# Performance work log

Hardware: AMD Instinct MI355X
Metric: run time of the kernel (lower is better)

## Reference

```python
import jax, jax.numpy as jnp
import numpy as np

# tinygemm asymmetric int4 convention
QUANT_MIN, QUANT_MAX = 0, 15
MID_POINT = (QUANT_MAX + QUANT_MIN + 1) / 2.0  # 8.0
OUT_F, IN_F, GROUP = 8192, 8192, 128
M_TOKENS = 64


def setup_inputs() -> dict:
    key = jax.random.key(0)
    kx, kw = jax.random.split(key)
    x = jax.random.normal(kx, (M_TOKENS, IN_F), dtype=jnp.float32)
    # Materialize quantized params exactly as quantize_weight_tinygemm does.
    w = jax.random.normal(kw, (OUT_F, IN_F), dtype=jnp.float32) * 0.02
    ng = IN_F // GROUP
    wg = w.reshape(OUT_F, ng, GROUP)
    min_val = wg.min(axis=2)
    max_val = wg.max(axis=2)
    scale = jnp.maximum((max_val - min_val) / float(QUANT_MAX - QUANT_MIN), 1.1920929e-7)
    zero_point = min_val + scale * MID_POINT
    min_val_recon = zero_point - scale * MID_POINT
    q = jnp.clip(jnp.round((wg - min_val_recon[..., None]) / scale[..., None]),
                 QUANT_MIN, QUANT_MAX).astype(jnp.int32)
    int_data = q.reshape(OUT_F, IN_F)  # values in [0, 15]
    # tinygemm layout: (n_groups, out_features, 2) with [..., 0]=scale, [..., 1]=zero_point
    scale_and_zero = jnp.stack([scale, zero_point], axis=-1).transpose(1, 0, 2)
    return {"x": x, "int_data": int_data, "scale_and_zero": scale_and_zero}


def reference(x, int_data, scale_and_zero):
    # Dequant: w = (q - MID_POINT) * scale + zero_point, per group of GROUP along in_features.
    ng = IN_F // GROUP
    q = int_data.reshape(OUT_F, ng, GROUP).astype(x.dtype)
    scale = scale_and_zero[..., 0].T[:, :, None]       # (OUT_F, ng, 1)
    zero_point = scale_and_zero[..., 1].T[:, :, None]  # (OUT_F, ng, 1)
    w = ((q - MID_POINT) * scale + zero_point).reshape(OUT_F, IN_F)
    return x @ w.T  # (M, OUT_F)
```

## Files before the change

kernel.cpp:

```cpp
#include <hip/hip_runtime.h>


#define OUT_F 8192
#define IN_F  8192
#define M_TOK 64
#define GROUP 128
#define BN    128
#define KSPLIT 16
#define KR    (IN_F / KSPLIT)

typedef short short8 __attribute__((ext_vector_type(8)));
typedef float f32x4  __attribute__((ext_vector_type(4)));
typedef int   int4v  __attribute__((ext_vector_type(4)));

__device__ __forceinline__ int pack_bf2(float lo, float hi) {
    unsigned ul = __float_as_uint(lo) + 0x8000u;
    unsigned uh = __float_as_uint(hi) + 0x8000u;
    return (int)((ul >> 16) | (uh & 0xFFFF0000u));
}

template <bool ATOMIC>
__global__ __launch_bounds__(256, 4)
void woq_gemm(const float* __restrict__ x,
              const int*   __restrict__ qw,
              const float* __restrict__ sz,
              float*       __restrict__ outp) {
    __shared__ int lds_x[16 * 64 * 4];

    const int t    = threadIdx.x;
    const int lane = t & 63;
    const int wv   = t >> 6;
    const int n0   = blockIdx.x * BN;
    const int k0   = blockIdx.y * KR;

    const int nlo  = lane & 15;
    const int quad = lane >> 4;
    const int kq8  = quad << 3;

    const int n1 = n0 + wv * 32 + nlo;
    const int n2 = n1 + 16;

    f32x4 acc[4][2];
#pragma unroll
    for (int mi = 0; mi < 4; ++mi)
#pragma unroll
        for (int ni = 0; ni < 2; ++ni)
            acc[mi][ni] = (f32x4){0.f, 0.f, 0.f, 0.f};

    for (int g = 0; g < KR / GROUP; ++g) {
        const int kg = k0 + g * GROUP;
        const int gg = kg >> 7;

        const float2 p1 = *(const float2*)(sz + ((size_t)gg * OUT_F + n1) * 2);
        const float2 p2 = *(const float2*)(sz + ((size_t)gg * OUT_F + n2) * 2);
        const float s1 = p1.x, c1 = fmaf(-8.f, p1.x, p1.y);
        const float s2 = p2.x, c2 = fmaf(-8.f, p2.x, p2.y);

        __syncthreads();
#pragma unroll
        for (int i = 0; i < 4; ++i) {
            int slot  = t + 256 * i;
            int chunk = slot >> 6;
            int l     = slot & 63;
            int m     = ((chunk & 3) << 4) + (l & 15);
            int kk    = ((chunk >> 2) << 5) + ((l >> 4) << 3);
            const float4* p = (const float4*)(x + (size_t)m * IN_F + kg + kk);
            float4 v0 = p[0];
            float4 v1 = p[1];
            int4v bv;
            bv.x = pack_bf2(v0.x, v0.y);
            bv.y = pack_bf2(v0.z, v0.w);
            bv.z = pack_bf2(v1.x, v1.y);
            bv.w = pack_bf2(v1.z, v1.w);
            *(int4v*)&lds_x[slot * 4] = bv;
        }
        __syncthreads();

#pragma unroll
        for (int ks = 0; ks < 4; ++ks) {
            const int k = kg + ks * 32;

            const int* q1p = qw + (size_t)n1 * IN_F + k + kq8;
            const int* q2p = qw + (size_t)n2 * IN_F + k + kq8;
            const int4 qa = *(const int4*)(q1p);
            const int4 qb = *(const int4*)(q1p + 4);
            const int4 qc = *(const int4*)(q2p);
            const int4 qd = *(const int4*)(q2p + 4);

            short8 a[4];
#pragma unroll
            for (int mi = 0; mi < 4; ++mi)
                a[mi] = *(const short8*)&lds_x[((ks * 4 + mi) * 64 + lane) * 4];

            int4v b1i, b2i;
            b1i.x = pack_bf2(fmaf((float)qa.x, s1, c1), fmaf((float)qa.y, s1, c1));
            b1i.y = pack_bf2(fmaf((float)qa.z, s1, c1), fmaf((float)qa.w, s1, c1));
            b1i.z = pack_bf2(fmaf((float)qb.x, s1, c1), fmaf((float)qb.y, s1, c1));
            b1i.w = pack_bf2(fmaf((float)qb.z, s1, c1), fmaf((float)qb.w, s1, c1));
            short8 b1 = __builtin_bit_cast(short8, b1i);
#pragma unroll
            for (int mi = 0; mi < 4; ++mi)
                acc[mi][0] = __builtin_amdgcn_mfma_f32_16x16x32_bf16(a[mi], b1, acc[mi][0], 0, 0, 0);

            b2i.x = pack_bf2(fmaf((float)qc.x, s2, c2), fmaf((float)qc.y, s2, c2));
            b2i.y = pack_bf2(fmaf((float)qc.z, s2, c2), fmaf((float)qc.w, s2, c2));
            b2i.z = pack_bf2(fmaf((float)qd.x, s2, c2), fmaf((float)qd.y, s2, c2));
            b2i.w = pack_bf2(fmaf((float)qd.z, s2, c2), fmaf((float)qd.w, s2, c2));
            short8 b2 = __builtin_bit_cast(short8, b2i);
#pragma unroll
            for (int mi = 0; mi < 4; ++mi)
                acc[mi][1] = __builtin_amdgcn_mfma_f32_16x16x32_bf16(a[mi], b2, acc[mi][1], 0, 0, 0);
        }
    }

    float* dst = ATOMIC ? outp : outp + (size_t)blockIdx.y * (M_TOK * OUT_F);
#pragma unroll
    for (int mi = 0; mi < 4; ++mi) {
#pragma unroll
        for (int ni = 0; ni < 2; ++ni) {
            const int n = n0 + wv * 32 + ni * 16 + nlo;
#pragma unroll
            for (int r = 0; r < 4; ++r) {
                const int m = mi * 16 + quad * 4 + r;
                if (ATOMIC)
                    atomicAdd(dst + (size_t)m * OUT_F + n, acc[mi][ni][r]);
                else
                    dst[(size_t)m * OUT_F + n] = acc[mi][ni][r];
            }
        }
    }
}

__global__ __launch_bounds__(256)
void woq_reduce(const float* __restrict__ part, float* __restrict__ out) {
    const int i = (blockIdx.x * 256 + threadIdx.x) * 4;
    const size_t stride = (size_t)M_TOK * OUT_F;
    float4 s = *(const float4*)(part + i);
#pragma unroll
    for (int k = 1; k < KSPLIT; ++k) {
        float4 v = *(const float4*)(part + (size_t)k * stride + i);
        s.x += v.x; s.y += v.y; s.z += v.z; s.w += v.w;
    }
    *(float4*)(out + i) = s;
}

extern "C" void kernel_launch(void* const* d_in, const int* in_sizes, int n_in,
                              void* d_out, int out_size, void* d_ws, size_t ws_size,
                              hipStream_t stream) {
    const float* x  = (const float*)d_in[0];
    const int*   qw = (const int*)d_in[1];
    const float* sz = (const float*)d_in[2];
    float* out = (float*)d_out;

    dim3 grid(OUT_F / BN, KSPLIT);
    const size_t need = (size_t)KSPLIT * M_TOK * OUT_F * sizeof(float);

    if (ws_size >= need) {
        float* part = (float*)d_ws;
        woq_gemm<false><<<grid, 256, 0, stream>>>(x, qw, sz, part);
        woq_reduce<<<(M_TOK * OUT_F) / (256 * 4), 256, 0, stream>>>(part, out);
    } else {
        hipMemsetAsync(d_out, 0, (size_t)out_size * sizeof(float), stream);
        woq_gemm<true><<<grid, 256, 0, stream>>>(x, qw, sz, out);
    }
}
```

Measured before the change: 390.4 us.

## Replace global split-K with in-block K split and LDS reduction

Drops the 16-way global split-K and its separate reduction kernel. Each 512-thread block now owns 32 output columns, and its 8 waves split as 2 M-halves by 4 K-quarters. The partial accumulators are combined through shared memory and written straight to the output. x is now read directly from global memory and converted to bf16 per wave instead of being staged through LDS. This removes the 32 MB partial-sum write and read and the second launch, but the grid shrinks to 256 blocks and x reads become redundant across blocks.

Measured after the change: 444.7 us. 1.14x slower.

```diff
diff --git a/kernel.cpp b/kernel.cpp
--- a/kernel.cpp
+++ b/kernel.cpp
@@ -5,9 +5,9 @@
 #define IN_F  8192
 #define M_TOK 64
 #define GROUP 128
-#define BN    128
-#define KSPLIT 16
-#define KR    (IN_F / KSPLIT)
+#define BN    32
+#define KW    4
+#define KR    (IN_F / KW)
 
 typedef short short8 __attribute__((ext_vector_type(8)));
 typedef float f32x4  __attribute__((ext_vector_type(4)));
@@ -19,36 +19,44 @@
     return (int)((ul >> 16) | (uh & 0xFFFF0000u));
 }
 
-template <bool ATOMIC>
-__global__ __launch_bounds__(256, 4)
+__global__ __launch_bounds__(512, 2)
 void woq_gemm(const float* __restrict__ x,
               const int*   __restrict__ qw,
               const float* __restrict__ sz,
               float*       __restrict__ outp) {
-    __shared__ int lds_x[16 * 64 * 4];
+    __shared__ f32x4 red[6 * 4 * 64];
 
     const int t    = threadIdx.x;
     const int lane = t & 63;
     const int wv   = t >> 6;
+    const int mh   = wv & 1;
+    const int kh   = wv >> 1;
     const int n0   = blockIdx.x * BN;
-    const int k0   = blockIdx.y * KR;
 
     const int nlo  = lane & 15;
     const int quad = lane >> 4;
     const int kq8  = quad << 3;
 
-    const int n1 = n0 + wv * 32 + nlo;
+    const int n1 = n0 + nlo;
     const int n2 = n1 + 16;
+    const int m0 = mh * 32;
 
-    f32x4 acc[4][2];
+    const float* xr0 = x  + (size_t)(m0 + nlo) * IN_F;
+    const float* xr1 = xr0 + (size_t)16 * IN_F;
+    const int*   qr1 = qw + (size_t)n1 * IN_F;
+    const int*   qr2 = qw + (size_t)n2 * IN_F;
+
+    f32x4 acc[2][2];
 #pragma unroll
-    for (int mi = 0; mi < 4; ++mi)
+    for (int mi = 0; mi < 2; ++mi)
 #pragma unroll
         for (int ni = 0; ni < 2; ++ni)
             acc[mi][ni] = (f32x4){0.f, 0.f, 0.f, 0.f};
 
+    const int kbase = kh * KR;
+
     for (int g = 0; g < KR / GROUP; ++g) {
-        const int kg = k0 + g * GROUP;
+        const int kg = kbase + g * GROUP;
         const int gg = kg >> 7;
 
         const float2 p1 = *(const float2*)(sz + ((size_t)gg * OUT_F + n1) * 2);
@@ -56,92 +64,82 @@
         const float s1 = p1.x, c1 = fmaf(-8.f, p1.x, p1.y);
         const float s2 = p2.x, c2 = fmaf(-8.f, p2.x, p2.y);
 
-        __syncthreads();
-#pragma unroll
-        for (int i = 0; i < 4; ++i) {
-            int slot  = t + 256 * i;
-            int chunk = slot >> 6;
-            int l     = slot & 63;
-            int m     = ((chunk & 3) << 4) + (l & 15);
-            int kk    = ((chunk >> 2) << 5) + ((l >> 4) << 3);
-            const float4* p = (const float4*)(x + (size_t)m * IN_F + kg + kk);
-            float4 v0 = p[0];
-            float4 v1 = p[1];
-            int4v bv;
-            bv.x = pack_bf2(v0.x, v0.y);
-            bv.y = pack_bf2(v0.z, v0.w);
-            bv.z = pack_bf2(v1.x, v1.y);
-            bv.w = pack_bf2(v1.z, v1.w);
-            *(int4v*)&lds_x[slot * 4] = bv;
-        }
-        __syncthreads();
-
 #pragma unroll
         for (int ks = 0; ks < 4; ++ks) {
-            const int k = kg + ks * 32;
+            const int k = kg + ks * 32 + kq8;
 
-            const int* q1p = qw + (size_t)n1 * IN_F + k + kq8;
-            const int* q2p = qw + (size_t)n2 * IN_F + k + kq8;
-            const int4 qa = *(const int4*)(q1p);
-            const int4 qb = *(const int4*)(q1p + 4);
-            const int4 qc = *(const int4*)(q2p);
-            const int4 qd = *(const int4*)(q2p + 4);
+            const int4 qa = *(const int4*)(qr1 + k);
+            const int4 qb = *(const int4*)(qr1 + k + 4);
+            const int4 qc = *(const int4*)(qr2 + k);
+            const int4 qd = *(const int4*)(qr2 + k + 4);
 
-            short8 a[4];
-#pragma unroll
-            for (int mi = 0; mi < 4; ++mi)
-                a[mi] = *(const short8*)&lds_x[((ks * 4 + mi) * 64 + lane) * 4];
+            const float4 va0 = *(const float4*)(xr0 + k);
+            const float4 va1 = *(const float4*)(xr0 + k + 4);
+            const float4 vb0 = *(const float4*)(xr1 + k);
+            const float4 vb1 = *(const float4*)(xr1 + k + 4);
+
+            int4v ai0, ai1;
+            ai0.x = pack_bf2(va0.x, va0.y);
+            ai0.y = pack_bf2(va0.z, va0.w);
+            ai0.z = pack_bf2(va1.x, va1.y);
+            ai0.w = pack_bf2(va1.z, va1.w);
+            ai1.x = pack_bf2(vb0.x, vb0.y);
+            ai1.y = pack_bf2(vb0.z, vb0.w);
+            ai1.z = pack_bf2(vb1.x, vb1.y);
+            ai1.w = pack_bf2(vb1.z, vb1.w);
+            const short8 a0 = __builtin_bit_cast(short8, ai0);
+            const short8 a1 = __builtin_bit_cast(short8, ai1);
 
             int4v b1i, b2i;
             b1i.x = pack_bf2(fmaf((float)qa.x, s1, c1), fmaf((float)qa.y, s1, c1));
             b1i.y = pack_bf2(fmaf((float)qa.z, s1, c1), fmaf((float)qa.w, s1, c1));
             b1i.z = pack_bf2(fmaf((float)qb.x, s1, c1), fmaf((float)qb.y, s1, c1));
             b1i.w = pack_bf2(fmaf((float)qb.z, s1, c1), fmaf((float)qb.w, s1, c1));
-            short8 b1 = __builtin_bit_cast(short8, b1i);
-#pragma unroll
-            for (int mi = 0; mi < 4; ++mi)
-                acc[mi][0] = __builtin_amdgcn_mfma_f32_16x16x32_bf16(a[mi], b1, acc[mi][0], 0, 0, 0);
-
             b2i.x = pack_bf2(fmaf((float)qc.x, s2, c2), fmaf((float)qc.y, s2, c2));
             b2i.y = pack_bf2(fmaf((float)qc.z, s2, c2), fmaf((float)qc.w, s2, c2));
             b2i.z = pack_bf2(fmaf((float)qd.x, s2, c2), fmaf((float)qd.y, s2, c2));
             b2i.w = pack_bf2(fmaf((float)qd.z, s2, c2), fmaf((float)qd.w, s2, c2));
-            short8 b2 = __builtin_bit_cast(short8, b2i);
-#pragma unroll
-            for (int mi = 0; mi < 4; ++mi)
-                acc[mi][1] = __builtin_amdgcn_mfma_f32_16x16x32_bf16(a[mi], b2, acc[mi][1], 0, 0, 0);
+            const short8 b1 = __builtin_bit_cast(short8, b1i);
+            const short8 b2 = __builtin_bit_cast(short8, b2i);
+
+            acc[0][0] = __builtin_amdgcn_mfma_f32_16x16x32_bf16(a0, b1, acc[0][0], 0, 0, 0);
+            acc[1][0] = __builtin_amdgcn_mfma_f32_16x16x32_bf16(a1, b1, acc[1][0], 0, 0, 0);
+            acc[0][1] = __builtin_amdgcn_mfma_f32_16x16x32_bf16(a0, b2, acc[0][1], 0, 0, 0);
+            acc[1][1] = __builtin_amdgcn_mfma_f32_16x16x32_bf16(a1, b2, acc[1][1], 0, 0, 0);
         }
     }
 
-    float* dst = ATOMIC ? outp : outp + (size_t)blockIdx.y * (M_TOK * OUT_F);
+    if (kh > 0) {
+        const int sb = ((kh - 1) * 2 + mh) * 4 * 64;
 #pragma unroll
-    for (int mi = 0; mi < 4; ++mi) {
+        for (int mi = 0; mi < 2; ++mi)
 #pragma unroll
-        for (int ni = 0; ni < 2; ++ni) {
-            const int n = n0 + wv * 32 + ni * 16 + nlo;
+            for (int ni = 0; ni < 2; ++ni)
+                red[sb + (mi * 2 + ni) * 64 + lane] = acc[mi][ni];
+    }
+    __syncthreads();
+    if (kh == 0) {
 #pragma unroll
-            for (int r = 0; r < 4; ++r) {
-                const int m = mi * 16 + quad * 4 + r;
-                if (ATOMIC)
-                    atomicAdd(dst + (size_t)m * OUT_F + n, acc[mi][ni][r]);
-                else
-                    dst[(size_t)m * OUT_F + n] = acc[mi][ni][r];
+        for (int p = 0; p < 3; ++p) {
+            const int sb = (p * 2 + mh) * 4 * 64;
+#pragma unroll
+            for (int mi = 0; mi < 2; ++mi)
+#pragma unroll
+                for (int ni = 0; ni < 2; ++ni)
+                    acc[mi][ni] += red[sb + (mi * 2 + ni) * 64 + lane];
+        }
+#pragma unroll
+        for (int mi = 0; mi < 2; ++mi)
+#pragma unroll
+            for (int ni = 0; ni < 2; ++ni) {
+                const int n = n0 + ni * 16 + nlo;
+#pragma unroll
+                for (int r = 0; r < 4; ++r) {
+                    const int m = m0 + mi * 16 + quad * 4 + r;
+                    outp[(size_t)m * OUT_F + n] = acc[mi][ni][r];
+                }
             }
-        }
     }
-}
-
-__global__ __launch_bounds__(256)
-void woq_reduce(const float* __restrict__ part, float* __restrict__ out) {
-    const int i = (blockIdx.x * 256 + threadIdx.x) * 4;
-    const size_t stride = (size_t)M_TOK * OUT_F;
-    float4 s = *(const float4*)(part + i);
-#pragma unroll
-    for (int k = 1; k < KSPLIT; ++k) {
-        float4 v = *(const float4*)(part + (size_t)k * stride + i);
-        s.x += v.x; s.y += v.y; s.z += v.z; s.w += v.w;
-    }
-    *(float4*)(out + i) = s;
 }
 
 extern "C" void kernel_launch(void* const* d_in, const int* in_sizes, int n_in,
@@ -152,15 +150,5 @@
     const float* sz = (const float*)d_in[2];
     float* out = (float*)d_out;
 
-    dim3 grid(OUT_F / BN, KSPLIT);
-    const size_t need = (size_t)KSPLIT * M_TOK * OUT_F * sizeof(float);
-
-    if (ws_size >= need) {
-        float* part = (float*)d_ws;
-        woq_gemm<false><<<grid, 256, 0, stream>>>(x, qw, sz, part);
-        woq_reduce<<<(M_TOK * OUT_F) / (256 * 4), 256, 0, stream>>>(part, out);
-    } else {
-        hipMemsetAsync(d_out, 0, (size_t)out_size * sizeof(float), stream);
-        woq_gemm<true><<<grid, 256, 0, stream>>>(x, qw, sz, out);
-    }
+    woq_gemm<<<dim3(OUT_F / BN), 512, 0, stream>>>(x, qw, sz, out);
 }
```
